# Performance work log

Measured on AMD Instinct MI355X. Metric: run time of the kernel, lower is better.

Reference implementation:

```python
import jax, jax.numpy as jnp
import numpy as np

B, S, D, H = 4, 2048, 1024, 16
HD = D // H  # head_dim = 64


def setup_inputs() -> dict:
    key = jax.random.key(0)
    ks = jax.random.split(key, 9)
    sd = 1.0 / np.sqrt(D)
    x = jax.random.normal(ks[0], (B, S, D), dtype=jnp.float32)
    Wq = jax.random.normal(ks[1], (D, D), dtype=jnp.float32) * sd
    Wk = jax.random.normal(ks[2], (D, D), dtype=jnp.float32) * sd
    Wv = jax.random.normal(ks[3], (D, D), dtype=jnp.float32) * sd
    Wo = jax.random.normal(ks[4], (D, D), dtype=jnp.float32) * sd
    bq = jax.random.normal(ks[5], (D,), dtype=jnp.float32) * sd
    bk = jax.random.normal(ks[6], (D,), dtype=jnp.float32) * sd
    bv = jax.random.normal(ks[7], (D,), dtype=jnp.float32) * sd
    bo = jax.random.normal(ks[8], (D,), dtype=jnp.float32) * sd
    return {"x": x, "Wq": Wq, "bq": bq, "Wk": Wk, "bk": bk,
            "Wv": Wv, "bv": bv, "Wo": Wo, "bo": bo}


def reference(x, Wq, bq, Wk, bk, Wv, bv, Wo, bo):
    b, s, d = x.shape
    scale = jnp.float32(np.sqrt(HD))
    # projections, split into heads: (b, h, s, hd)
    def heads(y):
        return y.reshape(b, s, H, HD).transpose(0, 2, 1, 3)
    Q = heads(x @ Wq + bq)
    K = heads(x @ Wk + bk)
    V = heads(x @ Wv + bv)
    # (b, h, s, s) scores with causal mask
    scores = jnp.einsum('bhqd,bhkd->bhqk', Q, K) / scale
    causal = jnp.tril(jnp.ones((s, s), dtype=bool))
    scores = jnp.where(causal[None, None], scores, jnp.float32(-jnp.inf))
    probs = jax.nn.softmax(scores, axis=-1)
    out = jnp.einsum('bhqk,bhkd->bhqd', probs, V)
    out = out.transpose(0, 2, 1, 3).reshape(b, s, d)
    return out @ Wo + bo
```

## Files before the change

kernel.cpp:

```cpp
#include <hip/hip_runtime.h>
#include <hip/hip_bf16.h>
#include <cstdint>

typedef __bf16 bf16x8 __attribute__((ext_vector_type(8)));
typedef float f32x4 __attribute__((ext_vector_type(4)));
typedef float f32x16 __attribute__((ext_vector_type(16)));
typedef unsigned short u16t;

__device__ __forceinline__ u16t f2bf(float f) {
    uint32_t u = __builtin_bit_cast(uint32_t, f);
    u += 0x7FFF + ((u >> 16) & 1);
    return (u16t)(u >> 16);
}

constexpr int Bb = 4, Ss = 2048, Dd = 1024, Hh = 16;
constexpr int Mrows = Bb * Ss;
constexpr float NEG = -1e30f;
constexpr float QSCALE = 0.125f * 1.44269504088896340736f;

__global__ __launch_bounds__(256) void cvt_bf16(const float* __restrict__ in,
                                                u16t* __restrict__ out, int n) {
    int i = (blockIdx.x * 256 + threadIdx.x) * 4;
    if (i >= n) return;
    float4 v = *(const float4*)(in + i);
    u16t o[4] = {f2bf(v.x), f2bf(v.y), f2bf(v.z), f2bf(v.w)};
    *(ushort4*)(out + i) = *(ushort4*)o;
}

__global__ __launch_bounds__(256) void transpose_cvt4(const float* __restrict__ W0,
                                                      const float* __restrict__ W1,
                                                      const float* __restrict__ W2,
                                                      const float* __restrict__ W3,
                                                      u16t* __restrict__ Tqkv,
                                                      u16t* __restrict__ To) {
    __shared__ float tile[64][65];
    int z = blockIdx.z;
    const float* W = z == 0 ? W0 : z == 1 ? W1 : z == 2 ? W2 : W3;
    u16t* WT = z < 3 ? Tqkv + (size_t)z * Dd * Dd : To;
    int n0 = blockIdx.x * 64, k0 = blockIdx.y * 64;
    int c = threadIdx.x & 63, r0 = (threadIdx.x >> 6) * 16;
    for (int i = 0; i < 16; i++)
        tile[c][r0 + i] = W[(size_t)(k0 + r0 + i) * Dd + n0 + c];
    __syncthreads();
    for (int i = 0; i < 16; i++)
        WT[(size_t)(n0 + r0 + i) * Dd + k0 + c] = f2bf(tile[r0 + i][c]);
}

#define GEMM_CORE_512(A_, BT_, m0_, n0_)                                                    \
    __shared__ __align__(16) u16t Asm3[3][128 * 64];                                        \
    __shared__ __align__(16) u16t Bsm3[3][256 * 64];                                        \
    int tid = threadIdx.x, lane = tid & 63, w = tid >> 6;                                   \
    int wm = w >> 2, wn = w & 3;                                                            \
    int ln = lane & 15, g = lane >> 4;                                                      \
    int l3 = lane >> 3, l7 = lane & 7;                                                      \
    int swz = (l7 ^ (l3 & 7)) * 8;                                                          \
    const u16t* Ap[2]; int Ao[2];                                                           \
    _Pragma("unroll")                                                                       \
    for (int ii = 0; ii < 2; ii++) {                                                        \
        int rg = m0_ + ii * 64 + w * 8 + l3;                                                \
        Ap[ii] = A_ + (size_t)rg * Dd + swz;                                                \
        Ao[ii] = ii * 4096 + w * 512;                                                       \
    }                                                                                       \
    const u16t* Bp[4]; int Bo[4];                                                           \
    _Pragma("unroll")                                                                       \
    for (int ii = 0; ii < 4; ii++) {                                                        \
        int rg = n0_ + ii * 64 + w * 8 + l3;                                                \
        Bp[ii] = BT_ + (size_t)rg * Dd + swz;                                               \
        Bo[ii] = ii * 4096 + w * 512;                                                       \
    }                                                                                       \
    auto stage = [&](int buf, int t) {                                                      \
        int k0 = t * 64;                                                                    \
        _Pragma("unroll")                                                                   \
        for (int ii = 0; ii < 2; ii++)                                                      \
            __builtin_amdgcn_global_load_lds(Ap[ii] + k0, &Asm3[buf][Ao[ii]], 16, 0, 0);    \
        _Pragma("unroll")                                                                   \
        for (int ii = 0; ii < 4; ii++)                                                      \
            __builtin_amdgcn_global_load_lds(Bp[ii] + k0, &Bsm3[buf][Bo[ii]], 16, 0, 0);    \
    };                                                                                      \
    f32x4 acc[4][4] = {};                                                                   \
    int coff[2] = {((g) ^ (ln & 7)) * 8, ((4 + g) ^ (ln & 7)) * 8};                         \
    int arow = wm * 64 + ln;                                                                \
    int brow = wn * 64 + ln;                                                                \
    auto compute = [&](int buf) {                                                           \
        bf16x8 af[4][2], bfr[4][2];                                                         \
        _Pragma("unroll")                                                                   \
        for (int i = 0; i < 4; i++)                                                         \
            _Pragma("unroll")                                                               \
            for (int ks = 0; ks < 2; ks++)                                                  \
                af[i][ks] = *(const bf16x8*)&Asm3[buf][(arow + i * 16) * 64 + coff[ks]];    \
        _Pragma("unroll")                                                                   \
        for (int j = 0; j < 4; j++)                                                         \
            _Pragma("unroll")                                                               \
            for (int ks = 0; ks < 2; ks++)                                                  \
                bfr[j][ks] = *(const bf16x8*)&Bsm3[buf][(brow + j * 16) * 64 + coff[ks]];   \
        _Pragma("unroll")                                                                   \
        for (int i = 0; i < 4; i++)                                                         \
            _Pragma("unroll")                                                               \
            for (int j = 0; j < 4; j++) {                                                   \
                acc[i][j] = __builtin_amdgcn_mfma_f32_16x16x32_bf16(af[i][0], bfr[j][0],    \
                                                                    acc[i][j], 0, 0, 0);    \
                acc[i][j] = __builtin_amdgcn_mfma_f32_16x16x32_bf16(af[i][1], bfr[j][1],    \
                                                                    acc[i][j], 0, 0, 0);    \
            }                                                                               \
    };                                                                                      \
    stage(0, 0);                                                                            \
    stage(1, 1);                                                                            \
    for (int t = 0; t < 14; t++) {                                                          \
        asm volatile("s_barrier" ::: "memory");                                             \
        stage((t + 2) % 3, t + 2);                                                          \
        asm volatile("s_waitcnt vmcnt(12)" ::: "memory");                                   \
        compute(t % 3);                                                                     \
    }                                                                                       \
    asm volatile("s_barrier" ::: "memory");                                                 \
    asm volatile("s_waitcnt vmcnt(6)" ::: "memory");                                        \
    compute(14 % 3);                                                                        \
    asm volatile("s_barrier" ::: "memory");                                                 \
    asm volatile("s_waitcnt vmcnt(0)" ::: "memory");                                        \
    compute(15 % 3);

__global__ __launch_bounds__(512) void gemm_qkv(const u16t* __restrict__ A,
                                                const u16t* __restrict__ BT,
                                                const float* __restrict__ bq,
                                                const float* __restrict__ bk,
                                                const float* __restrict__ bvv,
                                                u16t* __restrict__ Qh,
                                                u16t* __restrict__ Kh,
                                                u16t* __restrict__ Vt) {
    int bid = blockIdx.x;
    int wg = (bid & 7) * 96 + (bid >> 3);
    int m0 = (wg / 12) * 128, n0 = (wg % 12) * 256;

    GEMM_CORE_512(A, BT, m0, n0)

    #pragma unroll
    for (int i = 0; i < 4; i++) {
        #pragma unroll
        for (int j = 0; j < 4; j++) {
            int col = n0 + wn * 64 + j * 16 + ln;
            int seg = col >> 10, c1k = col & 1023;
            float bias = seg == 0 ? bq[c1k] : seg == 1 ? bk[c1k] : bvv[c1k];
            int rowb = m0 + wm * 64 + i * 16 + g * 4;
            int b = rowb >> 11, s = rowb & 2047, h = c1k >> 6, hd = c1k & 63;
            if (seg == 0) {
                for (int r = 0; r < 4; r++) {
                    float v = (acc[i][j][r] + bias) * QSCALE;
                    Qh[((size_t)(b * Hh + h) * Ss + s + r) * 64 + hd] = f2bf(v);
                }
            } else if (seg == 1) {
                for (int r = 0; r < 4; r++)
                    Kh[((size_t)(b * Hh + h) * Ss + s + r) * 64 + hd] = f2bf(acc[i][j][r] + bias);
            } else {
                u16t pk4[4];
                for (int r = 0; r < 4; r++) pk4[r] = f2bf(acc[i][j][r] + bias);
                *(ushort4*)(Vt + ((size_t)((b * Hh + h) * 64 + hd) << 11) + s) = *(ushort4*)pk4;
            }
        }
    }
}

__global__ __launch_bounds__(512) void gemm_o(const u16t* __restrict__ A,
                                              const u16t* __restrict__ BT,
                                              const float* __restrict__ bias,
                                              float* __restrict__ outF) {
    int bid = blockIdx.x;
    int wg = (bid & 7) * 32 + (bid >> 3);
    int m0 = (wg >> 2) * 128, n0 = (wg & 3) * 256;

    GEMM_CORE_512(A, BT, m0, n0)

    #pragma unroll
    for (int i = 0; i < 4; i++) {
        #pragma unroll
        for (int j = 0; j < 4; j++) {
            int col = n0 + wn * 64 + j * 16 + ln;
            float bv = bias[col];
            int rowb = m0 + wm * 64 + i * 16 + g * 4;
            for (int r = 0; r < 4; r++)
                outF[(size_t)(rowb + r) * Dd + col] = acc[i][j][r] + bv;
        }
    }
}

__global__ __launch_bounds__(512, 4) void attn(const u16t* __restrict__ Qh,
                                               const u16t* __restrict__ Kh,
                                               const u16t* __restrict__ Vt,
                                               u16t* __restrict__ Ob) {
    __shared__ __align__(16) u16t Ksm[2][2][64 * 64];
    __shared__ __align__(16) u16t Vsm[2][2][64 * 64];
    float*  mergeO  = (float*)&Ksm[0][0][0];
    float2* mergeML = (float2*)&Vsm[0][0][0];

    int tid = threadIdx.x, lane = tid & 63, w = tid >> 6;
    int grp = w >> 2, wg = w & 3;
    int l31 = lane & 31, hi = lane >> 5;
    int flat = blockIdx.y * 8 + blockIdx.x;
    int xcd = flat & 7, jj = flat >> 3;
    int bh = xcd * 8 + (jj >> 3);
    int ip = jj & 7;

    const u16t* Kb = Kh + (size_t)bh * Ss * 64;
    const u16t* Vb = Vt + (size_t)bh * 64 * Ss;

    int sr0 = wg * 16 + (lane >> 3);
    int sr1 = sr0 + 8;
    int sc0 = (((lane & 7) ^ (sr0 & 7) ^ ((sr0 >> 3) & 3)) * 8);
    int sc1 = (((lane & 7) ^ (sr1 & 7) ^ ((sr1 >> 3) & 3)) * 8);
    const u16t* Kg0 = Kb + (size_t)sr0 * 64 + sc0;
    const u16t* Kg1 = Kb + (size_t)sr1 * 64 + sc1;
    const u16t* Vg0 = Vb + (size_t)sr0 * Ss + sc0;
    const u16t* Vg1 = Vb + (size_t)sr1 * Ss + sc1;

    auto stage = [&](int buf, int t) {
        size_t koff = (size_t)t * 64 * 64;
        size_t voff = (size_t)t * 64;
        __builtin_amdgcn_global_load_lds(Kg0 + koff, &Ksm[grp][buf][(wg * 2 + 0) * 512], 16, 0, 0);
        __builtin_amdgcn_global_load_lds(Kg1 + koff, &Ksm[grp][buf][(wg * 2 + 1) * 512], 16, 0, 0);
        __builtin_amdgcn_global_load_lds(Vg0 + voff, &Vsm[grp][buf][(wg * 2 + 0) * 512], 16, 0, 0);
        __builtin_amdgcn_global_load_lds(Vg1 + voff, &Vsm[grp][buf][(wg * 2 + 1) * 512], 16, 0, 0);
    };

    int swzr = (l31 & 7) ^ ((l31 >> 3) & 3);

    for (int task = 0; task < 2; task++) {
        int qx = task == 0 ? ip : 15 - ip;
        int qb = qx * 128;
        int q0w = qb + wg * 32;
        int qlane = q0w + l31;

        bf16x8 qB[4];
        {
            const u16t* Qp = Qh + ((size_t)bh * Ss + qlane) * 64 + hi * 8;
            #pragma unroll
            for (int ks = 0; ks < 4; ks++)
                qB[ks] = *(const bf16x8*)(Qp + 16 * ks);
        }

        f32x16 oacc[2] = {};
        float m_run = NEG, l_run = 0.f;
        int half = qx + 1;
        int tbase = grp == 0 ? 0 : half;

        stage(0, tbase);
        __syncthreads();

        for (int it = 0; it < half; it++) {
            int cur = it & 1;
            int kv0 = (tbase + it) << 6;
            if (it + 1 < half) stage(cur ^ 1, tbase + it + 1);

            bool active = (kv0 <= q0w + 31);
            if (active) {
                f32x16 p0 = {}, p1 = {};
                __builtin_amdgcn_s_setprio(1);
                #pragma unroll
                for (int ks = 0; ks < 4; ks++) {
                    int cc = (2 * ks + hi) ^ swzr;
                    bf16x8 ka0 = *(const bf16x8*)&Ksm[grp][cur][(size_t)l31 * 64 + cc * 8];
                    bf16x8 ka1 = *(const bf16x8*)&Ksm[grp][cur][(size_t)(32 + l31) * 64 + cc * 8];
                    p0 = __builtin_amdgcn_mfma_f32_32x32x16_bf16(ka0, qB[ks], p0, 0, 0, 0);
                    p1 = __builtin_amdgcn_mfma_f32_32x32x16_bf16(ka1, qB[ks], p1, 0, 0, 0);
                }
                __builtin_amdgcn_s_setprio(0);

                if (kv0 + 63 > q0w) {
                    #pragma unroll
                    for (int r = 0; r < 16; r++) {
                        int kvg = kv0 + (r & 3) + 8 * (r >> 2) + 4 * hi;
                        if (kvg > qlane)      p0[r] = NEG;
                        if (kvg + 32 > qlane) p1[r] = NEG;
                    }
                }

                float ma = fmaxf(p0[0], p1[0]), mb = fmaxf(p0[1], p1[1]);
                float mc = fmaxf(p0[2], p1[2]), md = fmaxf(p0[3], p1[3]);
                #pragma unroll
                for (int r = 4; r < 16; r += 4) {
                    ma = fmaxf(ma, fmaxf(p0[r], p1[r]));
                    mb = fmaxf(mb, fmaxf(p0[r + 1], p1[r + 1]));
                    mc = fmaxf(mc, fmaxf(p0[r + 2], p1[r + 2]));
                    md = fmaxf(md, fmaxf(p0[r + 3], p1[r + 3]));
                }
                float mt = fmaxf(fmaxf(ma, mb), fmaxf(mc, md));
                mt = fmaxf(mt, __shfl_xor(mt, 32));
                if (__any(mt > m_run + 10.0f)) {
                    float mn = fmaxf(m_run, mt);
                    float al = __builtin_exp2f(m_run - mn);
                    m_run = mn;
                    l_run *= al;
                    #pragma unroll
                    for (int r = 0; r < 16; r++) { oacc[0][r] *= al; oacc[1][r] *= al; }
                }
                #pragma unroll
                for (int r = 0; r < 16; r++) {
                    p0[r] = __builtin_exp2f(p0[r] - m_run);
                    p1[r] = __builtin_exp2f(p1[r] - m_run);
                }
                float sa = 0.f, sb = 0.f, sc2 = 0.f, sd = 0.f;
                #pragma unroll
                for (int r = 0; r < 16; r += 4) {
                    sa += p0[r] + p1[r];
                    sb += p0[r + 1] + p1[r + 1];
                    sc2 += p0[r + 2] + p1[r + 2];
                    sd += p0[r + 3] + p1[r + 3];
                }
                float rsum = (sa + sb) + (sc2 + sd);
                rsum += __shfl_xor(rsum, 32);
                l_run += rsum;

                bf16x8 pb[4];
                {
                    uint32_t c0, c1, c2, c3;
                    asm("v_cvt_pk_bf16_f32 %0, %1, %2" : "=v"(c0) : "v"(p0[0]), "v"(p0[1]));
                    asm("v_cvt_pk_bf16_f32 %0, %1, %2" : "=v"(c1) : "v"(p0[2]), "v"(p0[3]));
                    asm("v_cvt_pk_bf16_f32 %0, %1, %2" : "=v"(c2) : "v"(p0[4]), "v"(p0[5]));
                    asm("v_cvt_pk_bf16_f32 %0, %1, %2" : "=v"(c3) : "v"(p0[6]), "v"(p0[7]));
                    asm volatile("v_permlane32_swap_b32 %0, %1" : "+v"(c0), "+v"(c2));
                    asm volatile("v_permlane32_swap_b32 %0, %1" : "+v"(c1), "+v"(c3));
                    uint32_t w4[4] = {c0, c1, c2, c3};
                    pb[0] = *(bf16x8*)w4;
                    uint32_t d0, d1, d2, d3;
                    asm("v_cvt_pk_bf16_f32 %0, %1, %2" : "=v"(d0) : "v"(p0[8]),  "v"(p0[9]));
                    asm("v_cvt_pk_bf16_f32 %0, %1, %2" : "=v"(d1) : "v"(p0[10]), "v"(p0[11]));
                    asm("v_cvt_pk_bf16_f32 %0, %1, %2" : "=v"(d2) : "v"(p0[12]), "v"(p0[13]));
                    asm("v_cvt_pk_bf16_f32 %0, %1, %2" : "=v"(d3) : "v"(p0[14]), "v"(p0[15]));
                    asm volatile("v_permlane32_swap_b32 %0, %1" : "+v"(d0), "+v"(d2));
                    asm volatile("v_permlane32_swap_b32 %0, %1" : "+v"(d1), "+v"(d3));
                    uint32_t w5[4] = {d0, d1, d2, d3};
                    pb[1] = *(bf16x8*)w5;
                    uint32_t e0, e1, e2, e3;
                    asm("v_cvt_pk_bf16_f32 %0, %1, %2" : "=v"(e0) : "v"(p1[0]), "v"(p1[1]));
                    asm("v_cvt_pk_bf16_f32 %0, %1, %2" : "=v"(e1) : "v"(p1[2]), "v"(p1[3]));
                    asm("v_cvt_pk_bf16_f32 %0, %1, %2" : "=v"(e2) : "v"(p1[4]), "v"(p1[5]));
                    asm("v_cvt_pk_bf16_f32 %0, %1, %2" : "=v"(e3) : "v"(p1[6]), "v"(p1[7]));
                    asm volatile("v_permlane32_swap_b32 %0, %1" : "+v"(e0), "+v"(e2));
                    asm volatile("v_permlane32_swap_b32 %0, %1" : "+v"(e1), "+v"(e3));
                    uint32_t w6[4] = {e0, e1, e2, e3};
                    pb[2] = *(bf16x8*)w6;
                    uint32_t f0, f1, f2, f3;
                    asm("v_cvt_pk_bf16_f32 %0, %1, %2" : "=v"(f0) : "v"(p1[8]),  "v"(p1[9]));
                    asm("v_cvt_pk_bf16_f32 %0, %1, %2" : "=v"(f1) : "v"(p1[10]), "v"(p1[11]));
                    asm("v_cvt_pk_bf16_f32 %0, %1, %2" : "=v"(f2) : "v"(p1[12]), "v"(p1[13]));
                    asm("v_cvt_pk_bf16_f32 %0, %1, %2" : "=v"(f3) : "v"(p1[14]), "v"(p1[15]));
                    asm volatile("v_permlane32_swap_b32 %0, %1" : "+v"(f0), "+v"(f2));
                    asm volatile("v_permlane32_swap_b32 %0, %1" : "+v"(f1), "+v"(f3));
                    uint32_t w7[4] = {f0, f1, f2, f3};
                    pb[3] = *(bf16x8*)w7;
                }

                __builtin_amdgcn_s_setprio(1);
                #pragma unroll
                for (int dt = 0; dt < 2; dt++) {
                    int drow = dt * 32 + l31;
                    #pragma unroll
                    for (int ks = 0; ks < 4; ks++) {
                        int cc = (2 * ks + hi) ^ swzr;
                        bf16x8 va = *(const bf16x8*)&Vsm[grp][cur][(size_t)drow * 64 + cc * 8];
                        oacc[dt] = __builtin_amdgcn_mfma_f32_32x32x16_bf16(va, pb[ks], oacc[dt], 0, 0, 0);
                    }
                }
                __builtin_amdgcn_s_setprio(0);
            }
            __syncthreads();
        }

        if (grp == 1) {
            if (hi == 0) {
                float2 v; v.x = m_run; v.y = l_run;
                mergeML[wg * 32 + l31] = v;
            }
            #pragma unroll
            for (int fidx = 0; fidx < 8; fidx++) {
                const int dt = fidx >> 2, rb = (fidx & 3) * 4;
                int fq = fidx ^ (l31 & 7);
                f32x4 ch;
                #pragma unroll
                for (int j = 0; j < 4; j++) ch[j] = oacc[dt][rb + j];
                *(f32x4*)(mergeO + ((size_t)(wg * 512 + l31 * 16 + hi * 8 + fq) << 2)) = ch;
            }
        }
        __syncthreads();

        if (grp == 0) {
            float2 ml1 = mergeML[wg * 32 + l31];
            float mmax = fmaxf(m_run, ml1.x);
            float e0 = __builtin_exp2f(m_run - mmax);
            float e1 = __builtin_exp2f(ml1.x - mmax);
            float linv = 1.0f / (l_run * e0 + ml1.y * e1);
            float f0 = e0 * linv, f1 = e1 * linv;
            #pragma unroll
            for (int fidx = 0; fidx < 8; fidx++) {
                const int dt = fidx >> 2, rb = (fidx & 3) * 4;
                int fq = fidx ^ (l31 & 7);
                f32x4 c1 = *(const f32x4*)(mergeO + ((size_t)(wg * 512 + l31 * 16 + hi * 8 + fq) << 2));
                #pragma unroll
                for (int j = 0; j < 4; j++)
                    oacc[dt][rb + j] = oacc[dt][rb + j] * f0 + c1[j] * f1;
            }
        }
        __syncthreads();

        if (grp == 0) {
            int b = bh >> 4, h = bh & 15;
            u16t* Op = Ob + ((size_t)(b * Ss + qlane)) * Dd + h * 64;
            #pragma unroll
            for (int dt = 0; dt < 2; dt++)
                #pragma unroll
                for (int rq = 0; rq < 4; rq++) {
                    u16t pk4[4];
                    #pragma unroll
                    for (int j = 0; j < 4; j++) pk4[j] = f2bf(oacc[dt][rq * 4 + j]);
                    int d0 = dt * 32 + rq * 8 + hi * 4;
                    *(ushort4*)(Op + d0) = *(ushort4*)pk4;
                }
        }
    }
}

extern "C" void kernel_launch(void* const* d_in, const int* in_sizes, int n_in,
                              void* d_out, int out_size, void* d_ws, size_t ws_size,
                              hipStream_t stream) {
    const float* x  = (const float*)d_in[0];
    const float* Wq = (const float*)d_in[1];
    const float* bq = (const float*)d_in[2];
    const float* Wk = (const float*)d_in[3];
    const float* bk = (const float*)d_in[4];
    const float* Wv = (const float*)d_in[5];
    const float* bv = (const float*)d_in[6];
    const float* Wo = (const float*)d_in[7];
    const float* bo = (const float*)d_in[8];

    char* ws = (char*)d_ws;
    size_t off = 0;
    auto alloc = [&](size_t bytes) { char* p = ws + off; off += (bytes + 255) & ~(size_t)255; return p; };
    u16t* xb    = (u16t*)alloc((size_t)Mrows * Dd * 2);
    u16t* WqkvT = (u16t*)alloc((size_t)3 * Dd * Dd * 2);
    u16t* WoT   = (u16t*)alloc((size_t)Dd * Dd * 2);
    u16t* Qh    = (u16t*)alloc((size_t)Mrows * Dd * 2);
    u16t* Kh    = (u16t*)alloc((size_t)Mrows * Dd * 2);
    u16t* Vtp   = (u16t*)alloc((size_t)Mrows * Dd * 2);
    u16t* Ob    = (u16t*)alloc((size_t)Mrows * Dd * 2);

    int nx = Mrows * Dd;
    cvt_bf16<<<nx / (256 * 4), 256, 0, stream>>>(x, xb, nx);
    dim3 tg(16, 16, 4);
    transpose_cvt4<<<tg, 256, 0, stream>>>(Wq, Wk, Wv, Wo, WqkvT, WoT);

    gemm_qkv<<<768, 512, 0, stream>>>(xb, WqkvT, bq, bk, bv, Qh, Kh, Vtp);

    dim3 ga(8, Bb * Hh);
    attn<<<ga, 512, 0, stream>>>(Qh, Kh, Vtp, Ob);

    gemm_o<<<256, 512, 0, stream>>>(Ob, WoT, bo, (float*)d_out);
}
```

Before: 192.5 us.

## Fuse input conversion into prep kernel and split GEMM k-step with setprio

```diff
diff --git a/kernel.cpp b/kernel.cpp
--- a/kernel.cpp
+++ b/kernel.cpp
@@ -18,32 +18,37 @@
 constexpr float NEG = -1e30f;
 constexpr float QSCALE = 0.125f * 1.44269504088896340736f;
 
-__global__ __launch_bounds__(256) void cvt_bf16(const float* __restrict__ in,
-                                                u16t* __restrict__ out, int n) {
-    int i = (blockIdx.x * 256 + threadIdx.x) * 4;
-    if (i >= n) return;
-    float4 v = *(const float4*)(in + i);
-    u16t o[4] = {f2bf(v.x), f2bf(v.y), f2bf(v.z), f2bf(v.w)};
-    *(ushort4*)(out + i) = *(ushort4*)o;
-}
-
-__global__ __launch_bounds__(256) void transpose_cvt4(const float* __restrict__ W0,
-                                                      const float* __restrict__ W1,
-                                                      const float* __restrict__ W2,
-                                                      const float* __restrict__ W3,
-                                                      u16t* __restrict__ Tqkv,
-                                                      u16t* __restrict__ To) {
+__global__ __launch_bounds__(256) void prep(const float* __restrict__ x,
+                                            u16t* __restrict__ xb,
+                                            const float* __restrict__ W0,
+                                            const float* __restrict__ W1,
+                                            const float* __restrict__ W2,
+                                            const float* __restrict__ W3,
+                                            u16t* __restrict__ Tqkv,
+                                            u16t* __restrict__ To) {
     __shared__ float tile[64][65];
     int z = blockIdx.z;
-    const float* W = z == 0 ? W0 : z == 1 ? W1 : z == 2 ? W2 : W3;
-    u16t* WT = z < 3 ? Tqkv + (size_t)z * Dd * Dd : To;
-    int n0 = blockIdx.x * 64, k0 = blockIdx.y * 64;
-    int c = threadIdx.x & 63, r0 = (threadIdx.x >> 6) * 16;
-    for (int i = 0; i < 16; i++)
-        tile[c][r0 + i] = W[(size_t)(k0 + r0 + i) * Dd + n0 + c];
-    __syncthreads();
-    for (int i = 0; i < 16; i++)
-        WT[(size_t)(n0 + r0 + i) * Dd + k0 + c] = f2bf(tile[r0 + i][c]);
+    if (z < 4) {
+        const float* W = z == 0 ? W0 : z == 1 ? W1 : z == 2 ? W2 : W3;
+        u16t* WT = z < 3 ? Tqkv + (size_t)z * Dd * Dd : To;
+        int n0 = blockIdx.x * 64, k0 = blockIdx.y * 64;
+        int c = threadIdx.x & 63, r0 = (threadIdx.x >> 6) * 16;
+        for (int i = 0; i < 16; i++)
+            tile[c][r0 + i] = W[(size_t)(k0 + r0 + i) * Dd + n0 + c];
+        __syncthreads();
+        for (int i = 0; i < 16; i++)
+            WT[(size_t)(n0 + r0 + i) * Dd + k0 + c] = f2bf(tile[r0 + i][c]);
+    } else {
+        int bid = blockIdx.y * 16 + blockIdx.x;
+        size_t base = (size_t)bid * 32768 + threadIdx.x * 4;
+        #pragma unroll 4
+        for (int it = 0; it < 32; it++) {
+            size_t i = base + (size_t)it * 1024;
+            float4 v = *(const float4*)(x + i);
+            u16t o[4] = {f2bf(v.x), f2bf(v.y), f2bf(v.z), f2bf(v.w)};
+            *(ushort4*)(xb + i) = *(ushort4*)o;
+        }
+    }
 }
 
 #define GEMM_CORE_512(A_, BT_, m0_, n0_)                                                    \
@@ -78,45 +83,45 @@
             __builtin_amdgcn_global_load_lds(Bp[ii] + k0, &Bsm3[buf][Bo[ii]], 16, 0, 0);    \
     };                                                                                      \
     f32x4 acc[4][4] = {};                                                                   \
-    int coff[2] = {((g) ^ (ln & 7)) * 8, ((4 + g) ^ (ln & 7)) * 8};                         \
+    int coff0 = ((g) ^ (ln & 7)) * 8;                                                       \
+    int coff1 = ((4 + g) ^ (ln & 7)) * 8;                                                   \
     int arow = wm * 64 + ln;                                                                \
     int brow = wn * 64 + ln;                                                                \
-    auto compute = [&](int buf) {                                                           \
-        bf16x8 af[4][2], bfr[4][2];                                                         \
+    auto compute_half = [&](int buf, int co) {                                              \
+        bf16x8 af[4], bfr[4];                                                               \
+        _Pragma("unroll")                                                                   \
+        for (int i = 0; i < 4; i++)                                                         \
+            af[i] = *(const bf16x8*)&Asm3[buf][(arow + i * 16) * 64 + co];                  \
+        _Pragma("unroll")                                                                   \
+        for (int j = 0; j < 4; j++)                                                         \
+            bfr[j] = *(const bf16x8*)&Bsm3[buf][(brow + j * 16) * 64 + co];                 \
+        __builtin_amdgcn_s_setprio(1);                                                      \
         _Pragma("unroll")                                                                   \
         for (int i = 0; i < 4; i++)                                                         \
             _Pragma("unroll")                                                               \
-            for (int ks = 0; ks < 2; ks++)                                                  \
-                af[i][ks] = *(const bf16x8*)&Asm3[buf][(arow + i * 16) * 64 + coff[ks]];    \
-        _Pragma("unroll")                                                                   \
-        for (int j = 0; j < 4; j++)                                                         \
-            _Pragma("unroll")                                                               \
-            for (int ks = 0; ks < 2; ks++)                                                  \
-                bfr[j][ks] = *(const bf16x8*)&Bsm3[buf][(brow + j * 16) * 64 + coff[ks]];   \
-        _Pragma("unroll")                                                                   \
-        for (int i = 0; i < 4; i++)                                                         \
-            _Pragma("unroll")                                                               \
-            for (int j = 0; j < 4; j++) {                                                   \
-                acc[i][j] = __builtin_amdgcn_mfma_f32_16x16x32_bf16(af[i][0], bfr[j][0],    \
+            for (int j = 0; j < 4; j++)                                                     \
+                acc[i][j] = __builtin_amdgcn_mfma_f32_16x16x32_bf16(af[i], bfr[j],          \
                                                                     acc[i][j], 0, 0, 0);    \
-                acc[i][j] = __builtin_amdgcn_mfma_f32_16x16x32_bf16(af[i][1], bfr[j][1],    \
-                                                                    acc[i][j], 0, 0, 0);    \
-            }                                                                               \
+        __builtin_amdgcn_s_setprio(0);                                                      \
     };                                                                                      \
     stage(0, 0);                                                                            \
     stage(1, 1);                                                                            \
+    asm volatile("s_waitcnt vmcnt(4)" ::: "memory");                                        \
     for (int t = 0; t < 14; t++) {                                                          \
         asm volatile("s_barrier" ::: "memory");                                             \
         stage((t + 2) % 3, t + 2);                                                          \
         asm volatile("s_waitcnt vmcnt(12)" ::: "memory");                                   \
-        compute(t % 3);                                                                     \
+        compute_half(t % 3, coff0);                                                         \
+        compute_half(t % 3, coff1);                                                         \
     }                                                                                       \
     asm volatile("s_barrier" ::: "memory");                                                 \
     asm volatile("s_waitcnt vmcnt(6)" ::: "memory");                                        \
-    compute(14 % 3);                                                                        \
+    compute_half(14 % 3, coff0);                                                            \
+    compute_half(14 % 3, coff1);                                                            \
     asm volatile("s_barrier" ::: "memory");                                                 \
     asm volatile("s_waitcnt vmcnt(0)" ::: "memory");                                        \
-    compute(15 % 3);
+    compute_half(15 % 3, coff0);                                                            \
+    compute_half(15 % 3, coff1);
 
 __global__ __launch_bounds__(512) void gemm_qkv(const u16t* __restrict__ A,
                                                 const u16t* __restrict__ BT,
@@ -440,10 +445,8 @@
     u16t* Vtp   = (u16t*)alloc((size_t)Mrows * Dd * 2);
     u16t* Ob    = (u16t*)alloc((size_t)Mrows * Dd * 2);
 
-    int nx = Mrows * Dd;
-    cvt_bf16<<<nx / (256 * 4), 256, 0, stream>>>(x, xb, nx);
-    dim3 tg(16, 16, 4);
-    transpose_cvt4<<<tg, 256, 0, stream>>>(Wq, Wk, Wv, Wo, WqkvT, WoT);
+    dim3 tg(16, 16, 5);
+    prep<<<tg, 256, 0, stream>>>(x, xb, Wq, Wk, Wv, Wo, WqkvT, WoT);
 
     gemm_qkv<<<768, 512, 0, stream>>>(xb, WqkvT, bq, bk, bv, Qh, Kh, Vtp);
 
```

After: 192.6 us. No clear change (+0.1%).
